# Optimization experiments

Measured on AMD Instinct MI355X. Metric: run time of the kernel, lower is better.

The kernel has to match this reference:

```python
import jax, jax.numpy as jnp
import numpy as np

EPS = 1e-8  # torch CosineSimilarity default eps

def _normalize(x):
    # torch clamps each norm at eps before dividing
    n = jnp.sqrt(jnp.sum(x * x, axis=-1, keepdims=True))
    return x / jnp.maximum(n, EPS)

def _cross_entropy(logits, labels):
    logp = jax.nn.log_softmax(logits, axis=-1)
    return -jnp.mean(jnp.take_along_axis(logp, labels[:, None], axis=-1))

def setup_inputs() -> dict:
    key = jax.random.key(0)
    ks = jax.random.split(key, 7)
    B, M, D = 8192, 3129, 512
    return {
        'mm_proj': jax.random.normal(ks[0], (B, D), jnp.float32),
        'ans_embedding': jax.random.normal(ks[1], (M, D), jnp.float32),
        'v_max': jax.random.normal(ks[2], (B, D), jnp.float32),
        'mm': jax.random.normal(ks[3], (B, D), jnp.float32),
        'logits_q': jax.random.normal(ks[4], (B, M), jnp.float32),
        'logits_rubi': jax.random.normal(ks[5], (B, M), jnp.float32),
        'class_id': jax.random.randint(ks[6], (B, 1), 0, M, jnp.int64),
    }

def reference(mm_proj, ans_embedding, v_max, mm, logits_q, logits_rubi, class_id,
              question_loss_weight=1.0):
    cid = class_id.squeeze(1)  # [B]
    # NCE over cosine similarities: fuse normalize + GEMM instead of [B,M,D] expand
    g = _normalize(mm_proj)          # [B, D]
    a = _normalize(ans_embedding)    # [M, D]
    d_logit = jnp.einsum('bd,md->bm', g, a)  # [B, M] cosine matrix
    positive_dist = jnp.take_along_axis(d_logit, cid[:, None], axis=1)[:, 0]  # [B]
    num = jnp.exp(positive_dist)
    den = jnp.sum(jnp.exp(d_logit), axis=-1)
    loss_nce = jnp.mean(-jnp.log(num / den))
    # object cosine loss
    obj_dist = jnp.sum(_normalize(v_max) * _normalize(mm), axis=-1)  # [B]
    obj_loss = jnp.mean(1.0 - obj_dist)
    fusion_loss = (_cross_entropy(logits_rubi, cid) + obj_loss + loss_nce) / 3.0
    question_loss = _cross_entropy(logits_q, cid)
    loss = fusion_loss + question_loss_weight * question_loss
    # out['loss'], out['loss_mm_q'], out['loss_q']
    return jnp.stack([loss, fusion_loss, question_loss])
```

## Files before the change

kernel.cpp:

```cpp
#include <hip/hip_runtime.h>
#include <hip/hip_bf16.h>

#define B_N 8192
#define M_N 3129
#define M_PAD 3200
#define D_N 512

#define GLOBAL_AS __attribute__((address_space(1)))
#define LDS_AS __attribute__((address_space(3)))

typedef __bf16 bf16x8 __attribute__((ext_vector_type(8)));
typedef float f32x4 __attribute__((ext_vector_type(4)));

__global__ __launch_bounds__(256) void normalize_kernel(
    const float* __restrict__ x, __bf16* __restrict__ y,
    int nrows_src, int nrows_out) {
  int wid = threadIdx.x >> 6, lane = threadIdx.x & 63;
  int row = blockIdx.x * 4 + wid;
  if (row >= nrows_out) return;
  bf16x8 out;
  if (row >= nrows_src) {
    for (int j = 0; j < 8; ++j) out[j] = (__bf16)0.0f;
    *(bf16x8*)(y + (size_t)row * D_N + lane * 8) = out;
    return;
  }
  const float4* xr = (const float4*)(x + (size_t)row * D_N);
  float4 v0 = xr[lane * 2], v1 = xr[lane * 2 + 1];
  float s = v0.x*v0.x + v0.y*v0.y + v0.z*v0.z + v0.w*v0.w
          + v1.x*v1.x + v1.y*v1.y + v1.z*v1.z + v1.w*v1.w;
  for (int o = 1; o < 64; o <<= 1) s += __shfl_xor(s, o);
  float rn = 1.0f / fmaxf(sqrtf(s), 1e-8f);
  float vals[8] = {v0.x, v0.y, v0.z, v0.w, v1.x, v1.y, v1.z, v1.w};
  for (int j = 0; j < 8; ++j) out[j] = (__bf16)(vals[j] * rn);
  *(bf16x8*)(y + (size_t)row * D_N + lane * 8) = out;
}

__global__ __launch_bounds__(256) void pos_kernel(
    const __bf16* __restrict__ g, const __bf16* __restrict__ a,
    const int* __restrict__ cid, float* __restrict__ pos) {
  int wid = threadIdx.x >> 6, lane = threadIdx.x & 63;
  int b = blockIdx.x * 4 + wid;
  if (b >= B_N) return;
  int label = cid[b];
  bf16x8 gv = *(const bf16x8*)(g + (size_t)b * D_N + lane * 8);
  bf16x8 av = *(const bf16x8*)(a + (size_t)label * D_N + lane * 8);
  float s = 0.0f;
  for (int j = 0; j < 8; ++j) s += (float)gv[j] * (float)av[j];
  for (int o = 1; o < 64; o <<= 1) s += __shfl_xor(s, o);
  if (lane == 0) pos[b] = s;
}

__global__ __launch_bounds__(256) void nce_gemm_kernel(
    const __bf16* __restrict__ g, const __bf16* __restrict__ a,
    float* __restrict__ den) {
  __shared__ __bf16 As[128 * 32];
  __shared__ __bf16 Bs[128 * 32];
  const int t = threadIdx.x;
  const int mtile = blockIdx.x;
  const int btile = blockIdx.y;
  const int brow0 = btile * 128;
  const int mrow0 = mtile * 128;
  const int lane = t & 63;
  const int wid = t >> 6;
  const int wrow = wid >> 1;
  const int wcol = wid & 1;
  const int r = lane & 15;
  const int quad = lane >> 4;

  f32x4 acc[4][4];
  for (int i = 0; i < 4; ++i)
    for (int j = 0; j < 4; ++j)
      acc[i][j] = f32x4{0.f, 0.f, 0.f, 0.f};

  for (int k0 = 0; k0 < D_N; k0 += 32) {
    __syncthreads();
    for (int i = 0; i < 2; ++i) {
      int s = t + i * 256;
      int row = s >> 2;
      int kq = (s & 3) << 3;
      const __bf16* ga = g + (size_t)(brow0 + row) * D_N + (k0 + kq);
      __builtin_amdgcn_global_load_lds((const GLOBAL_AS void*)ga,
                                       (LDS_AS void*)(As + s * 8), 16, 0, 0);
      const __bf16* gb = a + (size_t)(mrow0 + row) * D_N + (k0 + kq);
      __builtin_amdgcn_global_load_lds((const GLOBAL_AS void*)gb,
                                       (LDS_AS void*)(Bs + s * 8), 16, 0, 0);
    }
    __syncthreads();
    bf16x8 af[4], bf[4];
    for (int i = 0; i < 4; ++i)
      af[i] = *(const bf16x8*)(As + (wrow * 64 + i * 16 + r) * 32 + quad * 8);
    for (int j = 0; j < 4; ++j)
      bf[j] = *(const bf16x8*)(Bs + (wcol * 64 + j * 16 + r) * 32 + quad * 8);
    for (int i = 0; i < 4; ++i)
      for (int j = 0; j < 4; ++j)
        acc[i][j] = __builtin_amdgcn_mfma_f32_16x16x32_bf16(af[i], bf[j],
                                                            acc[i][j], 0, 0, 0);
  }

  for (int i = 0; i < 4; ++i) {
    for (int reg = 0; reg < 4; ++reg) {
      float s = 0.0f;
      for (int j = 0; j < 4; ++j) {
        int m = mrow0 + wcol * 64 + j * 16 + r;
        float v = acc[i][j][reg];
        if (m < M_N) s += __expf(v);
      }
      s += __shfl_xor(s, 1);
      s += __shfl_xor(s, 2);
      s += __shfl_xor(s, 4);
      s += __shfl_xor(s, 8);
      if (r == 0) {
        int b = brow0 + wrow * 64 + i * 16 + quad * 4 + reg;
        atomicAdd(den + b, s);
      }
    }
  }
}

__global__ __launch_bounds__(256) void obj_kernel(
    const float* __restrict__ v, const float* __restrict__ m,
    float* __restrict__ obj) {
  int wid = threadIdx.x >> 6, lane = threadIdx.x & 63;
  int b = blockIdx.x * 4 + wid;
  if (b >= B_N) return;
  const float4* vr = (const float4*)(v + (size_t)b * D_N);
  const float4* mr = (const float4*)(m + (size_t)b * D_N);
  float4 a0 = vr[lane * 2], a1 = vr[lane * 2 + 1];
  float4 b0 = mr[lane * 2], b1 = mr[lane * 2 + 1];
  float sv = a0.x*a0.x + a0.y*a0.y + a0.z*a0.z + a0.w*a0.w
           + a1.x*a1.x + a1.y*a1.y + a1.z*a1.z + a1.w*a1.w;
  float sm = b0.x*b0.x + b0.y*b0.y + b0.z*b0.z + b0.w*b0.w
           + b1.x*b1.x + b1.y*b1.y + b1.z*b1.z + b1.w*b1.w;
  float sd = a0.x*b0.x + a0.y*b0.y + a0.z*b0.z + a0.w*b0.w
           + a1.x*b1.x + a1.y*b1.y + a1.z*b1.z + a1.w*b1.w;
  for (int o = 1; o < 64; o <<= 1) {
    sv += __shfl_xor(sv, o);
    sm += __shfl_xor(sm, o);
    sd += __shfl_xor(sd, o);
  }
  if (lane == 0) {
    float dist = sd / (fmaxf(sqrtf(sv), 1e-8f) * fmaxf(sqrtf(sm), 1e-8f));
    obj[b] = 1.0f - dist;
  }
}

__global__ __launch_bounds__(256) void ce_kernel(
    const float* __restrict__ lq, const float* __restrict__ lr,
    const int* __restrict__ cid,
    float* __restrict__ ce_q, float* __restrict__ ce_r) {
  int b = blockIdx.x;
  const float* rq = lq + (size_t)b * M_N;
  const float* rr = lr + (size_t)b * M_N;
  int t = threadIdx.x;
  int mis = (int)(((size_t)b * M_N) & 3);
  int h = (4 - mis) & 3;
  int n4 = (M_N - h) >> 2;
  int tail0 = h + (n4 << 2);
  int ntail = M_N - tail0;
  float sq = 0.0f, sr = 0.0f;
  if (t < h) { sq += __expf(rq[t]); sr += __expf(rr[t]); }
  if (t >= 64 && t < 64 + ntail) {
    int i = tail0 + (t - 64);
    sq += __expf(rq[i]); sr += __expf(rr[i]);
  }
  const float4* q4 = (const float4*)(rq + h);
  const float4* r4 = (const float4*)(rr + h);
  for (int i = t; i < n4; i += 256) {
    float4 a = q4[i];
    float4 c = r4[i];
    sq += __expf(a.x) + __expf(a.y) + __expf(a.z) + __expf(a.w);
    sr += __expf(c.x) + __expf(c.y) + __expf(c.z) + __expf(c.w);
  }
  for (int o = 1; o < 64; o <<= 1) {
    sq += __shfl_xor(sq, o);
    sr += __shfl_xor(sr, o);
  }
  __shared__ float ssq[4], ssr[4];
  int wid = t >> 6;
  if ((t & 63) == 0) { ssq[wid] = sq; ssr[wid] = sr; }
  __syncthreads();
  if (t == 0) {
    float tq = ssq[0] + ssq[1] + ssq[2] + ssq[3];
    float tr = ssr[0] + ssr[1] + ssr[2] + ssr[3];
    int label = cid[b];
    ce_q[b] = logf(tq) - rq[label];
    ce_r[b] = logf(tr) - rr[label];
  }
}

__global__ __launch_bounds__(256) void final_kernel(
    const float* __restrict__ den, const float* __restrict__ pos,
    const float* __restrict__ ce_q, const float* __restrict__ ce_r,
    const float* __restrict__ obj, float* __restrict__ out) {
  int t = threadIdx.x;
  float s_nce = 0.0f, s_ceq = 0.0f, s_cer = 0.0f, s_obj = 0.0f;
  for (int b = t; b < B_N; b += 256) {
    s_nce += logf(den[b]) - pos[b];
    s_ceq += ce_q[b];
    s_cer += ce_r[b];
    s_obj += obj[b];
  }
  for (int o = 1; o < 64; o <<= 1) {
    s_nce += __shfl_xor(s_nce, o);
    s_ceq += __shfl_xor(s_ceq, o);
    s_cer += __shfl_xor(s_cer, o);
    s_obj += __shfl_xor(s_obj, o);
  }
  __shared__ float red[4][4];
  int wid = t >> 6;
  if ((t & 63) == 0) {
    red[wid][0] = s_nce; red[wid][1] = s_ceq;
    red[wid][2] = s_cer; red[wid][3] = s_obj;
  }
  __syncthreads();
  if (t == 0) {
    float nce = (red[0][0] + red[1][0] + red[2][0] + red[3][0]) / (float)B_N;
    float ceq = (red[0][1] + red[1][1] + red[2][1] + red[3][1]) / (float)B_N;
    float cer = (red[0][2] + red[1][2] + red[2][2] + red[3][2]) / (float)B_N;
    float ob  = (red[0][3] + red[1][3] + red[2][3] + red[3][3]) / (float)B_N;
    float fusion = (cer + ob + nce) * (1.0f / 3.0f);
    float loss = fusion + ceq;
    out[0] = loss;
    out[1] = fusion;
    out[2] = ceq;
  }
}

extern "C" void kernel_launch(void* const* d_in, const int* in_sizes, int n_in,
                              void* d_out, int out_size, void* d_ws, size_t ws_size,
                              hipStream_t stream) {
  const float* mm_proj     = (const float*)d_in[0];
  const float* ans_emb     = (const float*)d_in[1];
  const float* v_max       = (const float*)d_in[2];
  const float* mm          = (const float*)d_in[3];
  const float* logits_q    = (const float*)d_in[4];
  const float* logits_rubi = (const float*)d_in[5];
  const int*   cid         = (const int*)d_in[6];
  float* out = (float*)d_out;

  char* ws = (char*)d_ws;
  __bf16* g = (__bf16*)ws;
  __bf16* a = (__bf16*)(ws + 8388608);
  float* den  = (float*)(ws + 8388608 + 3276800);
  float* pos  = den + B_N;
  float* ce_q = pos + B_N;
  float* ce_r = ce_q + B_N;
  float* obj  = ce_r + B_N;

  hipMemsetAsync(den, 0, (size_t)B_N * sizeof(float), stream);

  normalize_kernel<<<B_N / 4, 256, 0, stream>>>(mm_proj, g, B_N, B_N);
  normalize_kernel<<<M_PAD / 4, 256, 0, stream>>>(ans_emb, a, M_N, M_PAD);
  pos_kernel<<<B_N / 4, 256, 0, stream>>>(g, a, cid, pos);
  nce_gemm_kernel<<<dim3(M_PAD / 128, B_N / 128), 256, 0, stream>>>(g, a, den);
  obj_kernel<<<B_N / 4, 256, 0, stream>>>(v_max, mm, obj);
  ce_kernel<<<B_N, 256, 0, stream>>>(logits_q, logits_rubi, cid, ce_q, ce_r);
  final_kernel<<<1, 256, 0, stream>>>(den, pos, ce_q, ce_r, obj, out);
}
```

Before: 340.2 us.

## Fuse prep kernels, extract positive logit in GEMM epilogue, unroll CE loads

Merges the two normalize launches and the object-cosine kernel into one prep kernel, and drops the separate positive-distance kernel by capturing the label's logit inside the NCE GEMM epilogue. The cross-entropy kernel now issues all float4 loads up front instead of looping, and computes row misalignment as b&3, which holds because M_N mod 4 is 1. This removes several launches and a re-read of the bf16 matrices, at the cost of a per-row cid load in the GEMM epilogue.

After: 340.8 us. Within noise of the previous version (+0.2%).

```diff
diff --git a/kernel.cpp b/kernel.cpp
--- a/kernel.cpp
+++ b/kernel.cpp
@@ -12,12 +12,13 @@
 typedef __bf16 bf16x8 __attribute__((ext_vector_type(8)));
 typedef float f32x4 __attribute__((ext_vector_type(4)));
 
-__global__ __launch_bounds__(256) void normalize_kernel(
+#define PREP_G_BLOCKS   (B_N / 4)
+#define PREP_A_BLOCKS   (M_PAD / 4)
+#define PREP_OBJ_BLOCKS (B_N / 4)
+
+__device__ __forceinline__ void normalize_row(
     const float* __restrict__ x, __bf16* __restrict__ y,
-    int nrows_src, int nrows_out) {
-  int wid = threadIdx.x >> 6, lane = threadIdx.x & 63;
-  int row = blockIdx.x * 4 + wid;
-  if (row >= nrows_out) return;
+    int row, int nrows_src, int lane) {
   bf16x8 out;
   if (row >= nrows_src) {
     for (int j = 0; j < 8; ++j) out[j] = (__bf16)0.0f;
@@ -35,24 +36,45 @@
   *(bf16x8*)(y + (size_t)row * D_N + lane * 8) = out;
 }
 
-__global__ __launch_bounds__(256) void pos_kernel(
-    const __bf16* __restrict__ g, const __bf16* __restrict__ a,
-    const int* __restrict__ cid, float* __restrict__ pos) {
+__global__ __launch_bounds__(256) void prep_kernel(
+    const float* __restrict__ mm_proj, const float* __restrict__ ans_emb,
+    const float* __restrict__ v_max, const float* __restrict__ mm,
+    __bf16* __restrict__ g, __bf16* __restrict__ a,
+    float* __restrict__ obj) {
+  int blk = blockIdx.x;
   int wid = threadIdx.x >> 6, lane = threadIdx.x & 63;
-  int b = blockIdx.x * 4 + wid;
-  if (b >= B_N) return;
-  int label = cid[b];
-  bf16x8 gv = *(const bf16x8*)(g + (size_t)b * D_N + lane * 8);
-  bf16x8 av = *(const bf16x8*)(a + (size_t)label * D_N + lane * 8);
-  float s = 0.0f;
-  for (int j = 0; j < 8; ++j) s += (float)gv[j] * (float)av[j];
-  for (int o = 1; o < 64; o <<= 1) s += __shfl_xor(s, o);
-  if (lane == 0) pos[b] = s;
+  if (blk < PREP_G_BLOCKS) {
+    normalize_row(mm_proj, g, blk * 4 + wid, B_N, lane);
+  } else if (blk < PREP_G_BLOCKS + PREP_A_BLOCKS) {
+    normalize_row(ans_emb, a, (blk - PREP_G_BLOCKS) * 4 + wid, M_N, lane);
+  } else {
+    int b = (blk - PREP_G_BLOCKS - PREP_A_BLOCKS) * 4 + wid;
+    const float4* vr = (const float4*)(v_max + (size_t)b * D_N);
+    const float4* mr = (const float4*)(mm + (size_t)b * D_N);
+    float4 a0 = vr[lane * 2], a1 = vr[lane * 2 + 1];
+    float4 b0 = mr[lane * 2], b1 = mr[lane * 2 + 1];
+    float sv = a0.x*a0.x + a0.y*a0.y + a0.z*a0.z + a0.w*a0.w
+             + a1.x*a1.x + a1.y*a1.y + a1.z*a1.z + a1.w*a1.w;
+    float sm = b0.x*b0.x + b0.y*b0.y + b0.z*b0.z + b0.w*b0.w
+             + b1.x*b1.x + b1.y*b1.y + b1.z*b1.z + b1.w*b1.w;
+    float sd = a0.x*b0.x + a0.y*b0.y + a0.z*b0.z + a0.w*b0.w
+             + a1.x*b1.x + a1.y*b1.y + a1.z*b1.z + a1.w*b1.w;
+    for (int o = 1; o < 64; o <<= 1) {
+      sv += __shfl_xor(sv, o);
+      sm += __shfl_xor(sm, o);
+      sd += __shfl_xor(sd, o);
+    }
+    if (lane == 0) {
+      float dist = sd / (fmaxf(sqrtf(sv), 1e-8f) * fmaxf(sqrtf(sm), 1e-8f));
+      obj[b] = 1.0f - dist;
+    }
+  }
 }
 
 __global__ __launch_bounds__(256) void nce_gemm_kernel(
     const __bf16* __restrict__ g, const __bf16* __restrict__ a,
-    float* __restrict__ den) {
+    const int* __restrict__ cid,
+    float* __restrict__ den, float* __restrict__ pos) {
   __shared__ __bf16 As[128 * 32];
   __shared__ __bf16 Bs[128 * 32];
   const int t = threadIdx.x;
@@ -99,48 +121,21 @@
 
   for (int i = 0; i < 4; ++i) {
     for (int reg = 0; reg < 4; ++reg) {
+      int b = brow0 + wrow * 64 + i * 16 + quad * 4 + reg;
+      int cid_b = cid[b];
       float s = 0.0f;
       for (int j = 0; j < 4; ++j) {
         int m = mrow0 + wcol * 64 + j * 16 + r;
         float v = acc[i][j][reg];
         if (m < M_N) s += __expf(v);
+        if (m == cid_b) pos[b] = v;
       }
       s += __shfl_xor(s, 1);
       s += __shfl_xor(s, 2);
       s += __shfl_xor(s, 4);
       s += __shfl_xor(s, 8);
-      if (r == 0) {
-        int b = brow0 + wrow * 64 + i * 16 + quad * 4 + reg;
-        atomicAdd(den + b, s);
-      }
-    }
-  }
-}
-
-__global__ __launch_bounds__(256) void obj_kernel(
-    const float* __restrict__ v, const float* __restrict__ m,
-    float* __restrict__ obj) {
-  int wid = threadIdx.x >> 6, lane = threadIdx.x & 63;
-  int b = blockIdx.x * 4 + wid;
-  if (b >= B_N) return;
-  const float4* vr = (const float4*)(v + (size_t)b * D_N);
-  const float4* mr = (const float4*)(m + (size_t)b * D_N);
-  float4 a0 = vr[lane * 2], a1 = vr[lane * 2 + 1];
-  float4 b0 = mr[lane * 2], b1 = mr[lane * 2 + 1];
-  float sv = a0.x*a0.x + a0.y*a0.y + a0.z*a0.z + a0.w*a0.w
-           + a1.x*a1.x + a1.y*a1.y + a1.z*a1.z + a1.w*a1.w;
-  float sm = b0.x*b0.x + b0.y*b0.y + b0.z*b0.z + b0.w*b0.w
-           + b1.x*b1.x + b1.y*b1.y + b1.z*b1.z + b1.w*b1.w;
-  float sd = a0.x*b0.x + a0.y*b0.y + a0.z*b0.z + a0.w*b0.w
-           + a1.x*b1.x + a1.y*b1.y + a1.z*b1.z + a1.w*b1.w;
-  for (int o = 1; o < 64; o <<= 1) {
-    sv += __shfl_xor(sv, o);
-    sm += __shfl_xor(sm, o);
-    sd += __shfl_xor(sd, o);
-  }
-  if (lane == 0) {
-    float dist = sd / (fmaxf(sqrtf(sv), 1e-8f) * fmaxf(sqrtf(sm), 1e-8f));
-    obj[b] = 1.0f - dist;
+      if (r == 0) atomicAdd(den + b, s);
+    }
   }
 }
 
@@ -152,24 +147,31 @@
   const float* rq = lq + (size_t)b * M_N;
   const float* rr = lr + (size_t)b * M_N;
   int t = threadIdx.x;
-  int mis = (int)(((size_t)b * M_N) & 3);
+  int mis = b & 3;
   int h = (4 - mis) & 3;
   int n4 = (M_N - h) >> 2;
   int tail0 = h + (n4 << 2);
   int ntail = M_N - tail0;
-  float sq = 0.0f, sr = 0.0f;
+  const float4* q4 = (const float4*)(rq + h);
+  const float4* r4 = (const float4*)(rr + h);
+  bool has3 = (t + 768) < n4;
+  int i3 = has3 ? (t + 768) : (n4 - 1);
+  float4 q0 = q4[t], q1 = q4[t + 256], q2 = q4[t + 512], q3 = q4[i3];
+  float4 p0 = r4[t], p1 = r4[t + 256], p2 = r4[t + 512], p3 = r4[i3];
+  float sq = __expf(q0.x) + __expf(q0.y) + __expf(q0.z) + __expf(q0.w)
+           + __expf(q1.x) + __expf(q1.y) + __expf(q1.z) + __expf(q1.w)
+           + __expf(q2.x) + __expf(q2.y) + __expf(q2.z) + __expf(q2.w);
+  float sr = __expf(p0.x) + __expf(p0.y) + __expf(p0.z) + __expf(p0.w)
+           + __expf(p1.x) + __expf(p1.y) + __expf(p1.z) + __expf(p1.w)
+           + __expf(p2.x) + __expf(p2.y) + __expf(p2.z) + __expf(p2.w);
+  if (has3) {
+    sq += __expf(q3.x) + __expf(q3.y) + __expf(q3.z) + __expf(q3.w);
+    sr += __expf(p3.x) + __expf(p3.y) + __expf(p3.z) + __expf(p3.w);
+  }
   if (t < h) { sq += __expf(rq[t]); sr += __expf(rr[t]); }
   if (t >= 64 && t < 64 + ntail) {
     int i = tail0 + (t - 64);
     sq += __expf(rq[i]); sr += __expf(rr[i]);
-  }
-  const float4* q4 = (const float4*)(rq + h);
-  const float4* r4 = (const float4*)(rr + h);
-  for (int i = t; i < n4; i += 256) {
-    float4 a = q4[i];
-    float4 c = r4[i];
-    sq += __expf(a.x) + __expf(a.y) + __expf(a.z) + __expf(a.w);
-    sr += __expf(c.x) + __expf(c.y) + __expf(c.z) + __expf(c.w);
   }
   for (int o = 1; o < 64; o <<= 1) {
     sq += __shfl_xor(sq, o);
@@ -249,11 +251,10 @@
 
   hipMemsetAsync(den, 0, (size_t)B_N * sizeof(float), stream);
 
-  normalize_kernel<<<B_N / 4, 256, 0, stream>>>(mm_proj, g, B_N, B_N);
-  normalize_kernel<<<M_PAD / 4, 256, 0, stream>>>(ans_emb, a, M_N, M_PAD);
-  pos_kernel<<<B_N / 4, 256, 0, stream>>>(g, a, cid, pos);
-  nce_gemm_kernel<<<dim3(M_PAD / 128, B_N / 128), 256, 0, stream>>>(g, a, den);
-  obj_kernel<<<B_N / 4, 256, 0, stream>>>(v_max, mm, obj);
+  prep_kernel<<<PREP_G_BLOCKS + PREP_A_BLOCKS + PREP_OBJ_BLOCKS, 256, 0,
+                stream>>>(mm_proj, ans_emb, v_max, mm, g, a, obj);
+  nce_gemm_kernel<<<dim3(M_PAD / 128, B_N / 128), 256, 0, stream>>>(
+      g, a, cid, den, pos);
   ce_kernel<<<B_N, 256, 0, stream>>>(logits_q, logits_rubi, cid, ce_q, ce_r);
   final_kernel<<<1, 256, 0, stream>>>(den, pos, ce_q, ce_r, obj, out);
 }
```
